# Kernel optimization log

Measured on AMD Instinct MI355X. Metric: run time of the kernel, lower is better.

The kernel has to match this reference:

```python
import jax, jax.numpy as jnp
import numpy as np

B, S, V, E, H, F, L = 64, 32, 10000, 512, 512, 2048, 2
D = E + H  # concat(x, h) size; embedding_size == hidden_size so all layers share shapes


def setup_inputs() -> dict:
    key = jax.random.key(0)
    ks = jax.random.split(key, 10)

    def w(k, shape, fan):
        return jax.random.normal(k, shape, jnp.float32) / jnp.sqrt(jnp.float32(fan))

    tokens = jax.random.randint(ks[0], (B, S), 0, V)
    cnn_features = jax.random.normal(ks[1], (B, F), jnp.float32)
    emb = w(ks[2], (V, E), E)
    w_in = w(ks[3], (F, H), F)
    b_in = jnp.zeros((H,), jnp.float32)
    w_r = w(ks[4], (L, D, H), D)
    b_r = jnp.zeros((L, 1, H), jnp.float32)
    w_u = w(ks[5], (L, D, H), D)
    b_u = jnp.zeros((L, 1, H), jnp.float32)
    w_h = w(ks[6], (L, D, H), D)
    b_h = jnp.zeros((L, 1, H), jnp.float32)
    w_out = w(ks[7], (H, V), H)
    b_out = jnp.zeros((V,), jnp.float32)
    return dict(tokens=tokens, cnn_features=cnn_features, emb=emb, w_in=w_in, b_in=b_in,
                w_r=w_r, b_r=b_r, w_u=w_u, b_u=b_u, w_h=w_h, b_h=b_h,
                w_out=w_out, b_out=b_out)


def reference(tokens, cnn_features, emb, w_in, b_in, w_r, b_r, w_u, b_u, w_h, b_h, w_out, b_out):
    x = emb[tokens]                                   # [B, S, E]
    h0 = cnn_features @ w_in + b_in                   # [B, H] initial hidden state from CNN features
    seq = x
    for l in range(L):
        Wr, br = w_r[l], b_r[l]
        Wu, bu = w_u[l], b_u[l]
        Wh, bh = w_h[l], b_h[l]

        def step(h, xt):
            # xt: [B, D_in], h: [B, H] -- same GRU math as GRUCell.forward, batched
            xh = jnp.concatenate([xt, h], axis=-1)
            r = jax.nn.sigmoid(xh @ Wr + br)
            h_tilde = jnp.tanh(jnp.concatenate([xt, r * h], axis=-1) @ Wh + bh)
            u = jax.nn.sigmoid(xh @ Wu + bu)
            h_new = h * u + (1.0 - u) * h_tilde
            return h_new, h_new

        _, ys = jax.lax.scan(step, h0, jnp.swapaxes(seq, 0, 1))  # scan over time
        seq = jnp.swapaxes(ys, 0, 1)                  # [B, S, H]
    logits = seq @ w_out + b_out                      # [B, S, V]
    return logits
```

## Files before the change

kernel.cpp:

```cpp
#include <hip/hip_runtime.h>
#include <hip/hip_bf16.h>

typedef __hip_bfloat16 bf16;
typedef __attribute__((ext_vector_type(8))) short bf16x8s;
typedef __attribute__((ext_vector_type(4))) float f32x4;
typedef __attribute__((ext_vector_type(4))) int i32x4;

#define NB 64
#define NS 32
#define NV 10000
#define NE 512
#define NH 512
#define NF 2048
#define ND 1024

static __device__ __forceinline__ float bf2f(bf16 x) { return __bfloat162float(x); }
static __device__ __forceinline__ bf16 f2bf(float x) { return __float2bfloat16(x); }
static __device__ __forceinline__ f32x4 mfma16(bf16x8s a, bf16x8s b, f32x4 c) {
  return __builtin_amdgcn_mfma_f32_16x16x32_bf16(a, b, c, 0, 0, 0);
}

static __device__ __forceinline__ i32x4 ld16_sc(const void* p) {
  i32x4 r;
  asm volatile("global_load_dwordx4 %0, %1, off sc0 sc1" : "=v"(r) : "v"(p) : "memory");
  return r;
}
static __device__ __forceinline__ void st16_sc(void* p, i32x4 v) {
  asm volatile("global_store_dwordx4 %0, %1, off sc0 sc1" :: "v"(p), "v"(v) : "memory");
}
static __device__ __forceinline__ void stud_sc(void* p, unsigned v) {
  asm volatile("global_store_dword %0, %1, off sc0 sc1" :: "v"(p), "v"(v) : "memory");
}
static __device__ __forceinline__ void wait_vm0() {
  asm volatile("s_waitcnt vmcnt(0)" ::: "memory");
  __builtin_amdgcn_sched_barrier(0);
}
static __device__ __forceinline__ unsigned min4u(i32x4 a) {
  return min(min((unsigned)a[0], (unsigned)a[1]), min((unsigned)a[2], (unsigned)a[3]));
}

__device__ __forceinline__ f32x4 wave_tile16(const bf16* A, const bf16* BT,
                                             int lda, int K, int m0, int n0) {
  int lane = threadIdx.x & 63;
  int r = lane & 15, g = lane >> 4;
  const bf16* ap = A + (size_t)(m0 + r) * lda + g * 8;
  const bf16* bp = BT + (size_t)(n0 + r) * K + g * 8;
  f32x4 acc = {0.f, 0.f, 0.f, 0.f};
#pragma unroll 4
  for (int k = 0; k < K; k += 32) {
    bf16x8s a = *(const bf16x8s*)(ap + k);
    bf16x8s b = *(const bf16x8s*)(bp + k);
    acc = mfma16(a, b, acc);
  }
  return acc;
}

__global__ void k_embed(const int* __restrict__ tokens, const float* __restrict__ emb,
                        bf16* __restrict__ x0) {
  int row = blockIdx.x;
  int tok = tokens[row];
  const float2* src = (const float2*)(emb + (size_t)tok * NE);
  uint32_t* dst = (uint32_t*)(x0 + (size_t)row * NE);
  float2 v = src[threadIdx.x];
  __hip_bfloat162 p;
  p.x = f2bf(v.x); p.y = f2bf(v.y);
  dst[threadIdx.x] = *(uint32_t*)&p;
}

__global__ void k_cvt(const float* __restrict__ src, bf16* __restrict__ dst, int n) {
  int i = blockIdx.x * 256 + threadIdx.x;
  if (i < n) dst[i] = f2bf(src[i]);
}

__global__ void k_transpose(const float* __restrict__ src, bf16* __restrict__ dst,
                            int K, int N) {
  __shared__ float tile[32][33];
  int n0 = blockIdx.x * 32, k0 = blockIdx.y * 32;
  int tx = threadIdx.x & 31, ty = threadIdx.x >> 5;
  for (int i = ty; i < 32; i += 8) {
    int k = k0 + i, n = n0 + tx;
    tile[i][tx] = (k < K && n < N) ? src[(size_t)k * N + n] : 0.f;
  }
  __syncthreads();
  for (int i = ty; i < 32; i += 8) {
    int n = n0 + i, k = k0 + tx;
    if (n < N && k < K) dst[(size_t)n * K + k] = f2bf(tile[tx][i]);
  }
}

__global__ void k_transpose12(const float* __restrict__ w_r, const float* __restrict__ w_u,
                              const float* __restrict__ w_h, bf16* __restrict__ ruhT,
                              bf16* __restrict__ hhT, bf16* __restrict__ xT) {
  int z = blockIdx.z, l = z / 6, q = z % 6;
  const float* srcs[6] = {
    w_r + (size_t)l * ND * NH + (size_t)512 * NH,
    w_u + (size_t)l * ND * NH + (size_t)512 * NH,
    w_h + (size_t)l * ND * NH + (size_t)512 * NH,
    w_r + (size_t)l * ND * NH,
    w_u + (size_t)l * ND * NH,
    w_h + (size_t)l * ND * NH };
  bf16* dsts[6] = {
    ruhT + (size_t)l * 1024 * 512,
    ruhT + (size_t)l * 1024 * 512 + 512 * 512,
    hhT  + (size_t)l * 512 * 512,
    xT   + (size_t)l * 1536 * 512,
    xT   + (size_t)l * 1536 * 512 + 512 * 512,
    xT   + (size_t)l * 1536 * 512 + 1024 * 512 };
  const float* src = srcs[q];
  bf16* dst = dsts[q];
  __shared__ float tile[32][33];
  int n0 = blockIdx.x * 32, k0 = blockIdx.y * 32;
  int tx = threadIdx.x & 31, ty = threadIdx.x >> 5;
  for (int i = ty; i < 32; i += 8)
    tile[i][tx] = src[(size_t)(k0 + i) * NH + n0 + tx];
  __syncthreads();
  for (int i = ty; i < 32; i += 8)
    dst[(size_t)(n0 + i) * NH + k0 + tx] = f2bf(tile[tx][i]);
}

__global__ void k_bias3all(const float* __restrict__ br, const float* __restrict__ bu,
                           const float* __restrict__ bh, float* __restrict__ bias) {
  int i = blockIdx.x * 256 + threadIdx.x;
  if (i < 3072) {
    int l = i / 1536, c = i % 1536;
    const float* s = (c < 512) ? (br + l * 512 + c)
                   : (c < 1024 ? (bu + l * 512 + (c - 512)) : (bh + l * 512 + (c - 1024)));
    bias[i] = *s;
  }
}

__global__ void k_gemm_h0(const bf16* __restrict__ A, const bf16* __restrict__ BT,
                          const float* __restrict__ bias,
                          float* __restrict__ h0f, bf16* __restrict__ h0b) {
  int wid = blockIdx.x * 4 + (threadIdx.x >> 6);
  int mt = wid & 3, nt = wid >> 2;
  f32x4 acc = wave_tile16(A, BT, NF, NF, mt * 16, nt * 16);
  int lane = threadIdx.x & 63;
  int cl = lane & 15, g = lane >> 4;
  int col = nt * 16 + cl;
  float bv = bias[col];
#pragma unroll
  for (int j = 0; j < 4; j++) {
    int row = mt * 16 + g * 4 + j;
    float v = acc[j] + bv;
    h0f[(size_t)row * NH + col] = v;
    h0b[(size_t)row * NH + col] = f2bf(v);
  }
}

__global__ __launch_bounds__(512, 1)
void k_gru2(const bf16* __restrict__ w_ruh, const bf16* __restrict__ w_hh,
            const bf16* __restrict__ w_x, const float* __restrict__ bias3,
            const float* __restrict__ h0f, const bf16* __restrict__ h0b,
            const bf16* __restrict__ x0, bf16* __restrict__ seq0,
            bf16* __restrict__ seq1, bf16* __restrict__ rh_all,
            float* __restrict__ pre, unsigned* __restrict__ flags,
            const bf16* __restrict__ w_out_T, const float* __restrict__ b_out,
            float* __restrict__ out) {
  __shared__ char lds[65536];
  const int tid = threadIdx.x;
  const int lane = tid & 63;
  const int wv = tid >> 6;
  const int cl = lane & 15, g4 = lane >> 4;
  const int bid = blockIdx.x;
  const int in0 = lane * 16;
  const int dsw = in0 ^ ((wv & 7) << 4);

  auto stage = [&](char* dst, const char* srcbase, int rstr) {
    i32x4 v0 = ld16_sc(srcbase + (size_t)wv * rstr + in0);
    i32x4 v1 = ld16_sc(srcbase + (size_t)(wv + 8) * rstr + in0);
    wait_vm0();
    *(i32x4*)(dst + wv * 1024 + dsw) = v0;
    *(i32x4*)(dst + (wv + 8) * 1024 + dsw) = v1;
  };
  auto afrag = [&](const char* panel, int kk) {
    return *(const bf16x8s*)(panel + cl * 1024 + ((kk * 64 + g4 * 16) ^ ((cl & 7) << 4)));
  };
  auto poll8 = [&](const unsigned* f, unsigned tgt) {
    if (tid == 0) {
      for (;;) {
        i32x4 a = ld16_sc(f);
        i32x4 b = ld16_sc(f + 4);
        wait_vm0();
        if (min(min4u(a), min4u(b)) >= tgt) break;
        __builtin_amdgcn_s_sleep(1);
      }
    }
    __syncthreads();
    __builtin_amdgcn_sched_barrier(0);
  };
  auto poll32 = [&](const unsigned* f, unsigned tgt) {
    if (tid == 0) {
      for (;;) {
        i32x4 a0 = ld16_sc(f),      a1 = ld16_sc(f + 4),  a2 = ld16_sc(f + 8),
              a3 = ld16_sc(f + 12), a4 = ld16_sc(f + 16), a5 = ld16_sc(f + 20),
              a6 = ld16_sc(f + 24), a7 = ld16_sc(f + 28);
        wait_vm0();
        unsigned mn = min(min(min(min4u(a0), min4u(a1)), min(min4u(a2), min4u(a3))),
                          min(min(min4u(a4), min4u(a5)), min(min4u(a6), min4u(a7))));
        if (mn >= tgt) break;
        __builtin_amdgcn_s_sleep(1);
      }
    }
    __syncthreads();
    __builtin_amdgcn_sched_barrier(0);
  };

  if (bid < 64) {
    const int l = bid >> 5, wg5 = bid & 31, mt = wg5 & 3, ng = wg5 >> 2;
    const bool is_u = (wv >= 4);
    const int wsub = wv & 3;
    const int c = (ng * 4 + wsub) * 16 + cl;
    const int colA = is_u ? 512 + c : c;
    char* hp = lds;
    char* rp = lds + 16384;
    float* ul = (float*)(lds + 32768);
    char* rout = lds + 36864;
    char* hout = lds + 38912;

    unsigned* f_h  = flags + (l * 4 + mt) * 32;
    unsigned* f_rh = flags + 256 + (l * 4 + mt) * 32;
    unsigned* f_pre = flags + 512 + (l * 4 + mt) * 32;

    bf16* seql = l ? seq1 : seq0;
    bf16* rh = rh_all + (size_t)l * 64 * 512;
    float* prel = pre + (size_t)l * 4 * 1536 * 64;

    bf16x8s bwA[16];
    { const bf16* pa = w_ruh + (size_t)l * 1024 * 512 + (size_t)colA * NH + g4 * 8;
#pragma unroll
      for (int k = 0; k < 16; k++) bwA[k] = *(const bf16x8s*)(pa + k * 32); }
    bf16x8s bwB[16];
    float h_reg[4];
    if (!is_u) {
      const bf16* pb = w_hh + (size_t)l * 512 * 512 + (size_t)c * NH + g4 * 8;
#pragma unroll
      for (int k = 0; k < 16; k++) bwB[k] = *(const bf16x8s*)(pb + k * 32);
#pragma unroll
      for (int j = 0; j < 4; j++)
        h_reg[j] = h0f[(size_t)(mt * 16 + g4 * 4 + j) * NH + c];
    }

    for (int t = 0; t < NS; t++) {
      if (tid == 0) {
        for (;;) {
          i32x4 p0 = ld16_sc(f_pre), p1 = ld16_sc(f_pre + 4), p2 = ld16_sc(f_pre + 8);
          i32x4 h0_, h1_;
          if (t) { h0_ = ld16_sc(f_h); h1_ = ld16_sc(f_h + 4); }
          wait_vm0();
          unsigned mnp = min(min(min4u(p0), min4u(p1)), min4u(p2));
          bool ok = mnp >= (unsigned)(t + 1);
          if (t) ok = ok && (min(min4u(h0_), min4u(h1_)) >= (unsigned)t);
          if (ok) break;
          __builtin_amdgcn_s_sleep(1);
        }
      }
      __syncthreads();
      __builtin_amdgcn_sched_barrier(0);
      const int slot = t & 3;
      i32x4 pv1 = ld16_sc(prel + ((size_t)(slot * 1536 + colA) * 64 + mt * 16 + g4 * 4));
      i32x4 pv2 = {0, 0, 0, 0};
      if (!is_u)
        pv2 = ld16_sc(prel + ((size_t)(slot * 1536 + 1024 + c) * 64 + mt * 16 + g4 * 4));
      if (t == 0) stage(hp, (const char*)(h0b + (size_t)mt * 16 * NH), 1024);
      else        stage(hp, (const char*)seql + ((size_t)(mt * 16) * NS + (t - 1)) * 1024,
                        NS * 1024);
      __syncthreads();
      f32x4 pA = *(f32x4*)&pv1;
      f32x4 pB = *(f32x4*)&pv2;
      {
        f32x4 acc = {0.f, 0.f, 0.f, 0.f};
#pragma unroll
        for (int kk = 0; kk < 16; kk++) acc = mfma16(afrag(hp, kk), bwA[kk], acc);
#pragma unroll
        for (int j = 0; j < 4; j++) {
          float gate = 1.f / (1.f + expf(-(acc[j] + pA[j])));
          if (is_u) {
            ul[(g4 * 4 + j) * 64 + wsub * 16 + cl] = gate;
          } else {
            bf16 o = f2bf(gate * h_reg[j]);
            *(unsigned short*)(rout + (g4 * 4 + j) * 128 + (wsub * 16 + cl) * 2)
              = *(unsigned short*)&o;
          }
        }
      }
      __syncthreads();
      {
        if (tid < 128) {
          int row = tid >> 3, ch = tid & 7;
          i32x4 v = *(i32x4*)(rout + row * 128 + ch * 16);
          st16_sc((char*)rh + (((size_t)(mt * 16 + row)) * NH + ng * 64 + ch * 8) * 2, v);
        }
        wait_vm0();
        __syncthreads();
        if (tid == 0) stud_sc(f_rh + ng, (unsigned)(t + 1));
      }
      poll8(f_rh, (unsigned)(t + 1));
      stage(rp, (const char*)(rh + (size_t)mt * 16 * NH), 1024);
      __syncthreads();
      if (!is_u) {
        f32x4 acc = {0.f, 0.f, 0.f, 0.f};
#pragma unroll
        for (int kk = 0; kk < 16; kk++) acc = mfma16(afrag(rp, kk), bwB[kk], acc);
#pragma unroll
        for (int j = 0; j < 4; j++) {
          float htil = tanhf(acc[j] + pB[j]);
          float u = ul[(g4 * 4 + j) * 64 + wsub * 16 + cl];
          float hnew = h_reg[j] * u + (1.f - u) * htil;
          h_reg[j] = hnew;
          bf16 hn = f2bf(hnew);
          *(unsigned short*)(hout + (g4 * 4 + j) * 128 + (wsub * 16 + cl) * 2)
            = *(unsigned short*)&hn;
        }
      }
      __syncthreads();
      {
        if (tid < 128) {
          int row = tid >> 3, ch = tid & 7;
          i32x4 v = *(i32x4*)(hout + row * 128 + ch * 16);
          st16_sc((char*)seql + (((size_t)(mt * 16 + row) * NS + t) * NH + ng * 64 + ch * 8) * 2, v);
        }
        wait_vm0();
        __syncthreads();
        if (tid == 0) {
          stud_sc(f_h + ng, (unsigned)(t + 1));
          if (l == 1) stud_sc(flags + 960 + mt * 8 + ng, (unsigned)(t + 1));
        }
      }
    }
  } else if (bid < 160) {
    const int wb = bid - 64;
    const int l = wb / 48, w48 = wb % 48, gg = w48 & 3, cw = w48 >> 2;
    char* xpan = lds;
    const int col = cw * 128 + wv * 16 + cl;
    const bf16* xsrc = l ? seq0 : x0;
    float* prel = pre + (size_t)l * 4 * 1536 * 64;
    unsigned* f_h0g = flags + (0 * 4 + gg) * 32;
    unsigned* f_own = flags + (l * 4 + gg) * 32;
    unsigned* f_out = flags + 512 + (l * 4 + gg) * 32 + cw;

    bf16x8s wxw[16];
    { const bf16* pw = w_x + (size_t)l * 1536 * 512 + (size_t)col * 512 + g4 * 8;
#pragma unroll
      for (int kk = 0; kk < 16; kk++) wxw[kk] = *(const bf16x8s*)(pw + kk * 32); }
    const float bz = bias3[l * 1536 + col];

    for (int t = 0; t < NS; t++) {
      if (l == 1 || t >= 4) {
        if (tid == 0) {
          for (;;) {
            i32x4 a0 = {0,0,0,0}, a1 = {0,0,0,0}, b0 = {0,0,0,0}, b1 = {0,0,0,0};
            if (l == 1) { a0 = ld16_sc(f_h0g); a1 = ld16_sc(f_h0g + 4); }
            if (t >= 4) { b0 = ld16_sc(f_own); b1 = ld16_sc(f_own + 4); }
            wait_vm0();
            bool ok = true;
            if (l == 1) ok = min(min4u(a0), min4u(a1)) >= (unsigned)(t + 1);
            if (t >= 4) ok = ok && (min(min4u(b0), min4u(b1)) >= (unsigned)(t - 3));
            if (ok) break;
            __builtin_amdgcn_s_sleep(1);
          }
        }
        __syncthreads();
        __builtin_amdgcn_sched_barrier(0);
      }
      stage(xpan, (const char*)xsrc + ((size_t)(gg * 16) * NS + t) * 1024, NS * 1024);
      __syncthreads();
      f32x4 acc = {0.f, 0.f, 0.f, 0.f};
#pragma unroll
      for (int kk = 0; kk < 16; kk++) acc = mfma16(afrag(xpan, kk), wxw[kk], acc);
      {
        f32x4 o;
#pragma unroll
        for (int j = 0; j < 4; j++) o[j] = acc[j] + bz;
        st16_sc(prel + ((size_t)((t & 3) * 1536 + col) * 64 + gg * 16 + g4 * 4),
                *(i32x4*)&o);
      }
      wait_vm0();
      __syncthreads();
      if (tid == 0) stud_sc(f_out, (unsigned)(t + 1));
    }
  } else {
    const int oj = bid - 160;
    char* aslab = lds;
    const int tile = oj * 8 + wv;
    const int colb = tile * 16 + cl;
    bf16x8s bwO[16];
    { const bf16* pw = w_out_T + (size_t)colb * 512 + g4 * 8;
#pragma unroll
      for (int kk = 0; kk < 16; kk++) bwO[kk] = *(const bf16x8s*)(pw + kk * 32); }
    const float bz = (colb < NV) ? b_out[colb] : 0.f;
    unsigned* f1 = flags + 960;

    for (int t = 0; t < NS; t++) {
      poll32(f1, (unsigned)(t + 1));
      {
        i32x4 vv[8];
        int rows[8], offs[8];
#pragma unroll
        for (int k8 = 0; k8 < 8; k8++) {
          int chunk = k8 * 512 + tid;
          rows[k8] = chunk >> 6;
          offs[k8] = (chunk & 63) * 16;
          vv[k8] = ld16_sc((const char*)seq1 + (size_t)t * 1024 +
                           (size_t)rows[k8] * (NS * 1024) + offs[k8]);
        }
        wait_vm0();
#pragma unroll
        for (int k8 = 0; k8 < 8; k8++)
          *(i32x4*)(aslab + rows[k8] * 1024 + (offs[k8] ^ ((rows[k8] & 7) << 4))) = vv[k8];
      }
      __syncthreads();
      f32x4 acc[4] = {};
#pragma unroll
      for (int kk = 0; kk < 16; kk++) {
#pragma unroll
        for (int mi = 0; mi < 4; mi++) {
          int row = mi * 16 + cl;
          bf16x8s a = *(const bf16x8s*)(aslab + row * 1024 +
                                        ((kk * 64 + g4 * 16) ^ ((row & 7) << 4)));
          acc[mi] = mfma16(a, bwO[kk], acc[mi]);
        }
      }
      if (colb < NV) {
#pragma unroll
        for (int mi = 0; mi < 4; mi++)
#pragma unroll
          for (int j = 0; j < 4; j++) {
            int b = mi * 16 + g4 * 4 + j;
            out[((size_t)b * NS + t) * NV + colb] = acc[mi][j] + bz;
          }
      }
      __syncthreads();
    }
  }
}

extern "C" void kernel_launch(void* const* d_in, const int* in_sizes, int n_in,
                              void* d_out, int out_size, void* d_ws, size_t ws_size,
                              hipStream_t stream) {
  const int*   tokens = (const int*)d_in[0];
  const float* cnn    = (const float*)d_in[1];
  const float* emb    = (const float*)d_in[2];
  const float* w_in   = (const float*)d_in[3];
  const float* b_in   = (const float*)d_in[4];
  const float* w_r    = (const float*)d_in[5];
  const float* b_r    = (const float*)d_in[6];
  const float* w_u    = (const float*)d_in[7];
  const float* b_u    = (const float*)d_in[8];
  const float* w_h    = (const float*)d_in[9];
  const float* b_h    = (const float*)d_in[10];
  const float* w_out  = (const float*)d_in[11];
  const float* b_out  = (const float*)d_in[12];
  float* out = (float*)d_out;

  char* ws = (char*)d_ws;
  size_t off = 0;
  auto alloc = [&](size_t bytes) { char* p = ws + off; off += (bytes + 255) & ~(size_t)255; return p; };
  bf16*  x0      = (bf16*) alloc((size_t)2048 * 512 * 2);
  bf16*  seq0    = (bf16*) alloc((size_t)2048 * 512 * 2);
  bf16*  seq1    = (bf16*) alloc((size_t)2048 * 512 * 2);
  float* pre     = (float*)alloc((size_t)2 * 4 * 1536 * 64 * 4);
  float* h0f     = (float*)alloc((size_t)64 * 512 * 4);
  bf16*  h0b     = (bf16*) alloc((size_t)64 * 512 * 2);
  bf16*  rh_all  = (bf16*) alloc((size_t)2 * 64 * 512 * 2);
  float* bias3   = (float*)alloc((size_t)2 * 1536 * 4);
  bf16*  cnn_b   = (bf16*) alloc((size_t)64 * 2048 * 2);
  bf16*  w_in_T  = (bf16*) alloc((size_t)512 * 2048 * 2);
  bf16*  w_ruh_T = (bf16*) alloc((size_t)2 * 1024 * 512 * 2);
  bf16*  w_hh_T  = (bf16*) alloc((size_t)2 * 512 * 512 * 2);
  bf16*  w_x_T   = (bf16*) alloc((size_t)2 * 1536 * 512 * 2);
  bf16*  w_out_T = (bf16*) alloc((size_t)12288 * 512 * 2);
  unsigned* flags = (unsigned*)alloc(4096);
  (void)ws_size; (void)in_sizes; (void)n_in; (void)out_size;

  hipMemsetAsync(flags, 0, 4096, stream);
  hipMemsetAsync(w_out_T + (size_t)10000 * 512, 0, (size_t)(12288 - 10000) * 512 * 2, stream);

  k_embed<<<2048, 256, 0, stream>>>(tokens, emb, x0);
  k_cvt<<<512, 256, 0, stream>>>(cnn, cnn_b, 64 * 2048);
  k_transpose<<<dim3(16, 64), 256, 0, stream>>>(w_in, w_in_T, NF, NH);
  k_transpose12<<<dim3(16, 16, 12), 256, 0, stream>>>(w_r, w_u, w_h, w_ruh_T, w_hh_T, w_x_T);
  k_transpose<<<dim3(313, 16), 256, 0, stream>>>(w_out, w_out_T, 512, NV);
  k_bias3all<<<12, 256, 0, stream>>>(b_r, b_u, b_h, bias3);

  k_gemm_h0<<<32, 256, 0, stream>>>(cnn_b, w_in_T, b_in, h0f, h0b);

  k_gru2<<<256, 512, 0, stream>>>(w_ruh_T, w_hh_T, w_x_T, bias3, h0f, h0b,
                                  x0, seq0, seq1, rh_all, pre, flags,
                                  w_out_T, b_out, out);
}
```

Before: 260.8 us.

## Fuse embedding gather and output-weight conversion into persistent GRU kernel

Removes the separate embedding kernel by having layer-0 input-projection blocks gather token embeddings and convert them to bf16 directly into LDS. Removes the w_out transpose kernel and its padding memset; output blocks instead load and convert fp32 w_out columns into registers themselves. Output blocks are retiled so each handles 32 batch rows by 32 columns rather than 64 rows by 16, and the LDS allocation shrinks. This cuts launches and an intermediate buffer, at the cost of strided uncoalesced fp32 weight reads in the output block prologue.

```diff
diff --git a/kernel.cpp b/kernel.cpp
--- a/kernel.cpp
+++ b/kernel.cpp
@@ -16,6 +16,7 @@
 
 static __device__ __forceinline__ float bf2f(bf16 x) { return __bfloat162float(x); }
 static __device__ __forceinline__ bf16 f2bf(float x) { return __float2bfloat16(x); }
+static __device__ __forceinline__ short bfbits(float x) { bf16 h = f2bf(x); return *(short*)&h; }
 static __device__ __forceinline__ f32x4 mfma16(bf16x8s a, bf16x8s b, f32x4 c) {
   return __builtin_amdgcn_mfma_f32_16x16x32_bf16(a, b, c, 0, 0, 0);
 }
@@ -53,18 +54,6 @@
     acc = mfma16(a, b, acc);
   }
   return acc;
-}
-
-__global__ void k_embed(const int* __restrict__ tokens, const float* __restrict__ emb,
-                        bf16* __restrict__ x0) {
-  int row = blockIdx.x;
-  int tok = tokens[row];
-  const float2* src = (const float2*)(emb + (size_t)tok * NE);
-  uint32_t* dst = (uint32_t*)(x0 + (size_t)row * NE);
-  float2 v = src[threadIdx.x];
-  __hip_bfloat162 p;
-  p.x = f2bf(v.x); p.y = f2bf(v.y);
-  dst[threadIdx.x] = *(uint32_t*)&p;
 }
 
 __global__ void k_cvt(const float* __restrict__ src, bf16* __restrict__ dst, int n) {
@@ -152,12 +141,12 @@
 void k_gru2(const bf16* __restrict__ w_ruh, const bf16* __restrict__ w_hh,
             const bf16* __restrict__ w_x, const float* __restrict__ bias3,
             const float* __restrict__ h0f, const bf16* __restrict__ h0b,
-            const bf16* __restrict__ x0, bf16* __restrict__ seq0,
-            bf16* __restrict__ seq1, bf16* __restrict__ rh_all,
-            float* __restrict__ pre, unsigned* __restrict__ flags,
-            const bf16* __restrict__ w_out_T, const float* __restrict__ b_out,
-            float* __restrict__ out) {
-  __shared__ char lds[65536];
+            const int* __restrict__ tokens, const float* __restrict__ emb,
+            bf16* __restrict__ seq0, bf16* __restrict__ seq1,
+            bf16* __restrict__ rh_all, float* __restrict__ pre,
+            unsigned* __restrict__ flags, const float* __restrict__ w_out,
+            const float* __restrict__ b_out, float* __restrict__ out) {
+  __shared__ char lds[40960];
   const int tid = threadIdx.x;
   const int lane = tid & 63;
   const int wv = tid >> 6;
@@ -333,7 +322,6 @@
     const int l = wb / 48, w48 = wb % 48, gg = w48 & 3, cw = w48 >> 2;
     char* xpan = lds;
     const int col = cw * 128 + wv * 16 + cl;
-    const bf16* xsrc = l ? seq0 : x0;
     float* prel = pre + (size_t)l * 4 * 1536 * 64;
     unsigned* f_h0g = flags + (0 * 4 + gg) * 32;
     unsigned* f_own = flags + (l * 4 + gg) * 32;
@@ -363,7 +351,22 @@
         __syncthreads();
         __builtin_amdgcn_sched_barrier(0);
       }
-      stage(xpan, (const char*)xsrc + ((size_t)(gg * 16) * NS + t) * 1024, NS * 1024);
+      if (l == 0) {
+#pragma unroll
+        for (int rr = 0; rr < 2; rr++) {
+          int r = wv + rr * 8;
+          int tok = tokens[(gg * 16 + r) * NS + t];
+          const float* ep = emb + (size_t)tok * NE + lane * 8;
+          f32x4 v0 = *(const f32x4*)ep;
+          f32x4 v1 = *(const f32x4*)(ep + 4);
+          bf16x8s o;
+#pragma unroll
+          for (int j = 0; j < 4; j++) { o[j] = bfbits(v0[j]); o[4 + j] = bfbits(v1[j]); }
+          *(i32x4*)(xpan + r * 1024 + dsw) = *(i32x4*)&o;
+        }
+      } else {
+        stage(xpan, (const char*)seq0 + ((size_t)(gg * 16) * NS + t) * 1024, NS * 1024);
+      }
       __syncthreads();
       f32x4 acc = {0.f, 0.f, 0.f, 0.f};
 #pragma unroll
@@ -381,54 +384,70 @@
     }
   } else {
     const int oj = bid - 160;
+    const int bh = oj & 1, cg = oj >> 1;
     char* aslab = lds;
-    const int tile = oj * 8 + wv;
-    const int colb = tile * 16 + cl;
-    bf16x8s bwO[16];
-    { const bf16* pw = w_out_T + (size_t)colb * 512 + g4 * 8;
-#pragma unroll
-      for (int kk = 0; kk < 16; kk++) bwO[kk] = *(const bf16x8s*)(pw + kk * 32); }
-    const float bz = (colb < NV) ? b_out[colb] : 0.f;
-    unsigned* f1 = flags + 960;
+    const int colb0 = (cg * 16 + wv * 2) * 16 + cl;
+    const int colb1 = colb0 + 16;
+    bf16x8s bw0[16], bw1[16];
+#pragma unroll
+    for (int kk = 0; kk < 16; kk++) {
+      bf16x8s f0, f1;
+#pragma unroll
+      for (int jj = 0; jj < 8; jj++) {
+        int k = kk * 32 + g4 * 8 + jj;
+        f0[jj] = (colb0 < NV) ? bfbits(w_out[(size_t)k * NV + colb0]) : (short)0;
+        f1[jj] = (colb1 < NV) ? bfbits(w_out[(size_t)k * NV + colb1]) : (short)0;
+      }
+      bw0[kk] = f0; bw1[kk] = f1;
+    }
+    const float bz0 = (colb0 < NV) ? b_out[colb0] : 0.f;
+    const float bz1 = (colb1 < NV) ? b_out[colb1] : 0.f;
+    unsigned* f1f = flags + 960;
 
     for (int t = 0; t < NS; t++) {
-      poll32(f1, (unsigned)(t + 1));
+      poll32(f1f, (unsigned)(t + 1));
       {
-        i32x4 vv[8];
-        int rows[8], offs[8];
-#pragma unroll
-        for (int k8 = 0; k8 < 8; k8++) {
-          int chunk = k8 * 512 + tid;
-          rows[k8] = chunk >> 6;
-          offs[k8] = (chunk & 63) * 16;
-          vv[k8] = ld16_sc((const char*)seq1 + (size_t)t * 1024 +
-                           (size_t)rows[k8] * (NS * 1024) + offs[k8]);
+        i32x4 vv[4];
+        int rows[4], offs[4];
+#pragma unroll
+        for (int k4 = 0; k4 < 4; k4++) {
+          int chunk = k4 * 512 + tid;
+          rows[k4] = chunk >> 6;
+          offs[k4] = (chunk & 63) * 16;
+          vv[k4] = ld16_sc((const char*)seq1 +
+                           ((size_t)(bh * 32 + rows[k4]) * NS + t) * 1024 + offs[k4]);
         }
         wait_vm0();
 #pragma unroll
-        for (int k8 = 0; k8 < 8; k8++)
-          *(i32x4*)(aslab + rows[k8] * 1024 + (offs[k8] ^ ((rows[k8] & 7) << 4))) = vv[k8];
-      }
-      __syncthreads();
-      f32x4 acc[4] = {};
+        for (int k4 = 0; k4 < 4; k4++)
+          *(i32x4*)(aslab + rows[k4] * 1024 + (offs[k4] ^ ((rows[k4] & 7) << 4))) = vv[k4];
+      }
+      __syncthreads();
+      f32x4 acc00 = {}, acc01 = {}, acc10 = {}, acc11 = {};
 #pragma unroll
       for (int kk = 0; kk < 16; kk++) {
-#pragma unroll
-        for (int mi = 0; mi < 4; mi++) {
-          int row = mi * 16 + cl;
-          bf16x8s a = *(const bf16x8s*)(aslab + row * 1024 +
-                                        ((kk * 64 + g4 * 16) ^ ((row & 7) << 4)));
-          acc[mi] = mfma16(a, bwO[kk], acc[mi]);
-        }
-      }
-      if (colb < NV) {
-#pragma unroll
-        for (int mi = 0; mi < 4; mi++)
-#pragma unroll
-          for (int j = 0; j < 4; j++) {
-            int b = mi * 16 + g4 * 4 + j;
-            out[((size_t)b * NS + t) * NV + colb] = acc[mi][j] + bz;
-          }
+        int r0 = cl, r1 = 16 + cl;
+        bf16x8s a0 = *(const bf16x8s*)(aslab + r0 * 1024 +
+                                       ((kk * 64 + g4 * 16) ^ ((r0 & 7) << 4)));
+        bf16x8s a1 = *(const bf16x8s*)(aslab + r1 * 1024 +
+                                       ((kk * 64 + g4 * 16) ^ ((r1 & 7) << 4)));
+        acc00 = mfma16(a0, bw0[kk], acc00);
+        acc01 = mfma16(a0, bw1[kk], acc01);
+        acc10 = mfma16(a1, bw0[kk], acc10);
+        acc11 = mfma16(a1, bw1[kk], acc11);
+      }
+#pragma unroll
+      for (int j = 0; j < 4; j++) {
+        int b0r = bh * 32 + g4 * 4 + j;
+        int b1r = b0r + 16;
+        if (colb0 < NV) {
+          out[((size_t)b0r * NS + t) * NV + colb0] = acc00[j] + bz0;
+          out[((size_t)b1r * NS + t) * NV + colb0] = acc10[j] + bz0;
+        }
+        if (colb1 < NV) {
+          out[((size_t)b0r * NS + t) * NV + colb1] = acc01[j] + bz1;
+          out[((size_t)b1r * NS + t) * NV + colb1] = acc11[j] + bz1;
+        }
       }
       __syncthreads();
     }
@@ -456,7 +475,6 @@
   char* ws = (char*)d_ws;
   size_t off = 0;
   auto alloc = [&](size_t bytes) { char* p = ws + off; off += (bytes + 255) & ~(size_t)255; return p; };
-  bf16*  x0      = (bf16*) alloc((size_t)2048 * 512 * 2);
   bf16*  seq0    = (bf16*) alloc((size_t)2048 * 512 * 2);
   bf16*  seq1    = (bf16*) alloc((size_t)2048 * 512 * 2);
   float* pre     = (float*)alloc((size_t)2 * 4 * 1536 * 64 * 4);
@@ -469,23 +487,19 @@
   bf16*  w_ruh_T = (bf16*) alloc((size_t)2 * 1024 * 512 * 2);
   bf16*  w_hh_T  = (bf16*) alloc((size_t)2 * 512 * 512 * 2);
   bf16*  w_x_T   = (bf16*) alloc((size_t)2 * 1536 * 512 * 2);
-  bf16*  w_out_T = (bf16*) alloc((size_t)12288 * 512 * 2);
   unsigned* flags = (unsigned*)alloc(4096);
   (void)ws_size; (void)in_sizes; (void)n_in; (void)out_size;
 
   hipMemsetAsync(flags, 0, 4096, stream);
-  hipMemsetAsync(w_out_T + (size_t)10000 * 512, 0, (size_t)(12288 - 10000) * 512 * 2, stream);
-
-  k_embed<<<2048, 256, 0, stream>>>(tokens, emb, x0);
+
   k_cvt<<<512, 256, 0, stream>>>(cnn, cnn_b, 64 * 2048);
   k_transpose<<<dim3(16, 64), 256, 0, stream>>>(w_in, w_in_T, NF, NH);
   k_transpose12<<<dim3(16, 16, 12), 256, 0, stream>>>(w_r, w_u, w_h, w_ruh_T, w_hh_T, w_x_T);
-  k_transpose<<<dim3(313, 16), 256, 0, stream>>>(w_out, w_out_T, 512, NV);
   k_bias3all<<<12, 256, 0, stream>>>(b_r, b_u, b_h, bias3);
 
   k_gemm_h0<<<32, 256, 0, stream>>>(cnn_b, w_in_T, b_in, h0f, h0b);
 
   k_gru2<<<256, 512, 0, stream>>>(w_ruh_T, w_hh_T, w_x_T, bias3, h0f, h0b,
-                                  x0, seq0, seq1, rh_all, pre, flags,
-                                  w_out_T, b_out, out);
-}
+                                  tokens, emb, seq0, seq1, rh_all, pre, flags,
+                                  w_out, b_out, out);
+}
```

After: 238.9 us. 1.09x faster.
